# Kernel optimization log

Hardware: AMD Instinct MI355X
Metric: run time of the kernel (lower is better)

The kernel has to match this reference:

```python
import jax, jax.numpy as jnp
import numpy as np

NEG = -1000000000.0  # mask sentinel used by the torch module

def setup_inputs() -> dict:
    key = jax.random.key(0)
    k1, k2, k3, k4 = jax.random.split(key, 4)
    B, N, F_in, F_out = 8, 2048, 128, 64
    h = jax.random.normal(k1, (B, N, F_in), dtype=jnp.float32)
    adj_mask = jnp.where(jax.random.uniform(k2, (B, N, N)) < 0.7, 0.0, NEG).astype(jnp.float32)
    # xavier_uniform with gain=1.414
    g = 1.414
    limW = g * np.sqrt(6.0 / (F_in + F_out))
    W = jax.random.uniform(k3, (F_in, F_out), minval=-limW, maxval=limW, dtype=jnp.float32)
    lima = g * np.sqrt(6.0 / (2 * F_out + 1))
    a = jax.random.uniform(k4, (2 * F_out, 1), minval=-lima, maxval=lima, dtype=jnp.float32)
    return {"h": h, "adj_mask": adj_mask, "W": W, "a": a}

def reference(h, adj_mask, W, a):
    F_out = W.shape[1]
    wh = jnp.matmul(h, W)                       # [B, N, F_out]
    wh1 = jnp.matmul(wh, a[:F_out])             # [B, N, 1]
    wh2 = jnp.matmul(wh, a[F_out:])             # [B, N, 1]
    e = wh1 + jnp.swapaxes(wh2, 1, 2)           # [B, N, N] additive score
    e = jax.nn.leaky_relu(e, negative_slope=0.2)
    e = jnp.where(adj_mask == NEG, NEG, e)
    attention = jax.nn.softmax(e, axis=-1)      # dropout is identity in eval mode
    h_prime = jnp.matmul(attention, wh)         # [B, N, F_out]
    return jax.nn.elu(h_prime)
```

## Files before the change

### kernel.cpp

```cpp
#include <hip/hip_runtime.h>
#include <hip/hip_bf16.h>

#define BATCH 8
#define NN 2048
#define FIN 128
#define FOUT 64
#define ROWS_TOTAL (BATCH * NN)

typedef __attribute__((ext_vector_type(8))) short bf16x8;
typedef __attribute__((ext_vector_type(4))) float f32x4;
typedef __attribute__((ext_vector_type(8))) short short8;

__device__ inline short f2bf(float x) {
    __hip_bfloat16 b = __float2bfloat16(x);
    short s;
    __builtin_memcpy(&s, &b, 2);
    return s;
}

__device__ inline bf16x8 score8(float q, float4 w0, float4 w1, float4 a0, float4 a1) {
    float p[8];
    float e;
    e = q + w0.x; p[0] = __expf(fmaxf(e, 0.2f * e) + a0.x);
    e = q + w0.y; p[1] = __expf(fmaxf(e, 0.2f * e) + a0.y);
    e = q + w0.z; p[2] = __expf(fmaxf(e, 0.2f * e) + a0.z);
    e = q + w0.w; p[3] = __expf(fmaxf(e, 0.2f * e) + a0.w);
    e = q + w1.x; p[4] = __expf(fmaxf(e, 0.2f * e) + a1.x);
    e = q + w1.y; p[5] = __expf(fmaxf(e, 0.2f * e) + a1.y);
    e = q + w1.z; p[6] = __expf(fmaxf(e, 0.2f * e) + a1.z);
    e = q + w1.w; p[7] = __expf(fmaxf(e, 0.2f * e) + a1.w);
    bf16x8 r;
    #pragma unroll
    for (int i = 0; i < 8; ++i) r[i] = f2bf(p[i]);
    return r;
}

__global__ __launch_bounds__(256) void k1_proj(
        const float* __restrict__ h, const float* __restrict__ W,
        const float* __restrict__ a,
        short* __restrict__ whT, float* __restrict__ wh1, float* __restrict__ wh2) {
    const int tid  = threadIdx.x;
    const int lane = tid & 63;
    const int wid  = tid >> 6;
    const int gw   = blockIdx.x * 4 + wid;
    const int row0 = gw * 8;
    const int b    = row0 >> 11;
    const int rloc = row0 & (NN - 1);

    float acc[8] = {0.f,0.f,0.f,0.f,0.f,0.f,0.f,0.f};
    const float* hrow = h + (size_t)row0 * FIN;

    #pragma unroll 2
    for (int kc = 0; kc < FIN / 4; ++kc) {
        float wv0 = W[(4*kc + 0) * FOUT + lane];
        float wv1 = W[(4*kc + 1) * FOUT + lane];
        float wv2 = W[(4*kc + 2) * FOUT + lane];
        float wv3 = W[(4*kc + 3) * FOUT + lane];
        #pragma unroll
        for (int r = 0; r < 8; ++r) {
            float4 h4 = *(const float4*)(hrow + r * FIN + 4*kc);
            acc[r] = fmaf(h4.x, wv0, acc[r]);
            acc[r] = fmaf(h4.y, wv1, acc[r]);
            acc[r] = fmaf(h4.z, wv2, acc[r]);
            acc[r] = fmaf(h4.w, wv3, acc[r]);
        }
    }

    short8 st;
    #pragma unroll
    for (int r = 0; r < 8; ++r) st[r] = f2bf(acc[r]);
    *(short8*)(whT + ((size_t)b * FOUT + lane) * NN + rloc) = st;

    const float a1 = a[lane];
    const float a2 = a[FOUT + lane];
    #pragma unroll
    for (int r = 0; r < 8; ++r) {
        const int row = row0 + r;
        float v1 = acc[r] * a1;
        float v2 = acc[r] * a2;
        #pragma unroll
        for (int m = 32; m >= 1; m >>= 1) {
            v1 += __shfl_xor(v1, m, 64);
            v2 += __shfl_xor(v2, m, 64);
        }
        if (lane == 0) { wh1[row] = v1; wh2[row] = v2; }
    }
}

__global__ __launch_bounds__(256) void k2_attn(
        const float* __restrict__ adj, const short* __restrict__ whT,
        const float* __restrict__ wh1, const float* __restrict__ wh2,
        float* __restrict__ out) {
    __shared__ float lds_acc[4][16][FOUT];
    __shared__ float lds_l[4][16];

    const int tid  = threadIdx.x;
    const int lane = tid & 63;
    const int w    = tid >> 6;
    const int row0 = blockIdx.x * 16;
    const int b    = row0 >> 11;
    const int iloc = lane & 15;
    const int koff = (lane >> 4) * 8;

    const float* adjrow = adj + (size_t)(row0 + iloc) * NN;
    const float* wh2b   = wh2 + b * NN;
    const short* whTb   = whT + (size_t)b * FOUT * NN;
    const float  wh1v   = wh1[row0 + iloc];

    bf16x8 onesf, idxf;
    #pragma unroll
    for (int e = 0; e < 8; ++e) { onesf[e] = (short)0x3F80; idxf[e] = f2bf((float)iloc); }
    f32x4 rowM = {}, colM = {};
    rowM = __builtin_amdgcn_mfma_f32_16x16x32_bf16(idxf, onesf, rowM, 0, 0, 0);
    colM = __builtin_amdgcn_mfma_f32_16x16x32_bf16(onesf, idxf, colM, 0, 0, 0);
    int rmap[4], cmap[4];
    #pragma unroll
    for (int reg = 0; reg < 4; ++reg) {
        int r = (int)(rowM[reg] * 0.03125f + 0.5f);
        int c = (int)(colM[reg] * 0.03125f + 0.5f);
        rmap[reg] = min(max(r, 0), 15);
        cmap[reg] = min(max(c, 0), 15);
    }

    f32x4 acc[4] = {};
    f32x4 accl = {};

    const int base = w * 32 + koff;

    float4 aA0 = *(const float4*)(adjrow + base);
    float4 aA1 = *(const float4*)(adjrow + base + 4);
    float4 aB0 = *(const float4*)(adjrow + base + 128);
    float4 aB1 = *(const float4*)(adjrow + base + 132);
    float4 wA0 = *(const float4*)(wh2b + base);
    float4 wA1 = *(const float4*)(wh2b + base + 4);
    float4 wB0 = *(const float4*)(wh2b + base + 128);
    float4 wB1 = *(const float4*)(wh2b + base + 132);

    #pragma unroll
    for (int k = 0; k < 8; ++k) {
        const int jA = base + k * 256;
        const int jB = jA + 128;

        bf16x8 bfA[4], bfB[4];
        #pragma unroll
        for (int ft = 0; ft < 4; ++ft) {
            const short* rp = whTb + (size_t)(ft * 16 + iloc) * NN;
            bfA[ft] = *(const bf16x8*)(rp + jA);
            bfB[ft] = *(const bf16x8*)(rp + jB);
        }

        float4 naA0 = aA0, naA1 = aA1, naB0 = aB0, naB1 = aB1;
        float4 nwA0 = wA0, nwA1 = wA1, nwB0 = wB0, nwB1 = wB1;
        if (k < 7) {
            const float* qA = adjrow + jA + 256;
            const float* qW = wh2b + jA + 256;
            naA0 = *(const float4*)(qA);
            naA1 = *(const float4*)(qA + 4);
            naB0 = *(const float4*)(qA + 128);
            naB1 = *(const float4*)(qA + 132);
            nwA0 = *(const float4*)(qW);
            nwA1 = *(const float4*)(qW + 4);
            nwB0 = *(const float4*)(qW + 128);
            nwB1 = *(const float4*)(qW + 132);
        }

        bf16x8 afA = score8(wh1v, wA0, wA1, aA0, aA1);
        bf16x8 afB = score8(wh1v, wB0, wB1, aB0, aB1);

        accl = __builtin_amdgcn_mfma_f32_16x16x32_bf16(afA, onesf, accl, 0, 0, 0);
        #pragma unroll
        for (int ft = 0; ft < 4; ++ft)
            acc[ft] = __builtin_amdgcn_mfma_f32_16x16x32_bf16(afA, bfA[ft], acc[ft], 0, 0, 0);
        accl = __builtin_amdgcn_mfma_f32_16x16x32_bf16(afB, onesf, accl, 0, 0, 0);
        #pragma unroll
        for (int ft = 0; ft < 4; ++ft)
            acc[ft] = __builtin_amdgcn_mfma_f32_16x16x32_bf16(afB, bfB[ft], acc[ft], 0, 0, 0);

        aA0 = naA0; aA1 = naA1; aB0 = naB0; aB1 = naB1;
        wA0 = nwA0; wA1 = nwA1; wB0 = nwB0; wB1 = nwB1;
    }

    #pragma unroll
    for (int ft = 0; ft < 4; ++ft)
        #pragma unroll
        for (int reg = 0; reg < 4; ++reg)
            lds_acc[w][rmap[reg]][ft * 16 + cmap[reg]] = acc[ft][reg];
    #pragma unroll
    for (int reg = 0; reg < 4; ++reg)
        if (cmap[reg] == 0) lds_l[w][rmap[reg]] = accl[reg];
    __syncthreads();

    const int f  = tid & 63;
    const int r0 = tid >> 6;
    #pragma unroll
    for (int rr = 0; rr < 4; ++rr) {
        const int r = r0 * 4 + rr;
        float s = lds_acc[0][r][f] + lds_acc[1][r][f] + lds_acc[2][r][f] + lds_acc[3][r][f];
        float l = lds_l[0][r] + lds_l[1][r] + lds_l[2][r] + lds_l[3][r];
        float v = s / l;
        out[(size_t)(row0 + r) * FOUT + f] = (v > 0.f) ? v : (__expf(v) - 1.f);
    }
}

extern "C" void kernel_launch(void* const* d_in, const int* in_sizes, int n_in,
                              void* d_out, int out_size, void* d_ws, size_t ws_size,
                              hipStream_t stream) {
    const float* h   = (const float*)d_in[0];
    const float* adj = (const float*)d_in[1];
    const float* W   = (const float*)d_in[2];
    const float* a   = (const float*)d_in[3];
    float* out = (float*)d_out;

    short* whT = (short*)d_ws;
    float* wh1 = (float*)(whT + (size_t)BATCH * FOUT * NN);
    float* wh2 = wh1 + ROWS_TOTAL;

    k1_proj<<<ROWS_TOTAL / 32, 256, 0, stream>>>(h, W, a, whT, wh1, wh2);
    k2_attn<<<ROWS_TOTAL / 16, 256, 0, stream>>>(adj, whT, wh1, wh2, out);
}
```

Before: 73.85 us.

## Split attention K-loop across eight waves per block instead of four

```diff
diff --git a/kernel.cpp b/kernel.cpp
--- a/kernel.cpp
+++ b/kernel.cpp
@@ -87,12 +87,12 @@
     }
 }
 
-__global__ __launch_bounds__(256) void k2_attn(
+__global__ __launch_bounds__(512, 4) void k2_attn(
         const float* __restrict__ adj, const short* __restrict__ whT,
         const float* __restrict__ wh1, const float* __restrict__ wh2,
         float* __restrict__ out) {
-    __shared__ float lds_acc[4][16][FOUT];
-    __shared__ float lds_l[4][16];
+    __shared__ float lds_acc[8][16][FOUT];
+    __shared__ float lds_l[8][16];
 
     const int tid  = threadIdx.x;
     const int lane = tid & 63;
@@ -127,57 +127,36 @@
 
     const int base = w * 32 + koff;
 
-    float4 aA0 = *(const float4*)(adjrow + base);
-    float4 aA1 = *(const float4*)(adjrow + base + 4);
-    float4 aB0 = *(const float4*)(adjrow + base + 128);
-    float4 aB1 = *(const float4*)(adjrow + base + 132);
-    float4 wA0 = *(const float4*)(wh2b + base);
-    float4 wA1 = *(const float4*)(wh2b + base + 4);
-    float4 wB0 = *(const float4*)(wh2b + base + 128);
-    float4 wB1 = *(const float4*)(wh2b + base + 132);
+    float4 a0 = *(const float4*)(adjrow + base);
+    float4 a1 = *(const float4*)(adjrow + base + 4);
+    float4 w0 = *(const float4*)(wh2b + base);
+    float4 w1 = *(const float4*)(wh2b + base + 4);
 
     #pragma unroll
     for (int k = 0; k < 8; ++k) {
-        const int jA = base + k * 256;
-        const int jB = jA + 128;
-
-        bf16x8 bfA[4], bfB[4];
-        #pragma unroll
-        for (int ft = 0; ft < 4; ++ft) {
-            const short* rp = whTb + (size_t)(ft * 16 + iloc) * NN;
-            bfA[ft] = *(const bf16x8*)(rp + jA);
-            bfB[ft] = *(const bf16x8*)(rp + jB);
-        }
-
-        float4 naA0 = aA0, naA1 = aA1, naB0 = aB0, naB1 = aB1;
-        float4 nwA0 = wA0, nwA1 = wA1, nwB0 = wB0, nwB1 = wB1;
+        const int j0 = base + k * 256;
+
+        bf16x8 bf[4];
+        #pragma unroll
+        for (int ft = 0; ft < 4; ++ft)
+            bf[ft] = *(const bf16x8*)(whTb + (size_t)(ft * 16 + iloc) * NN + j0);
+
+        float4 na0 = a0, na1 = a1, nw0 = w0, nw1 = w1;
         if (k < 7) {
-            const float* qA = adjrow + jA + 256;
-            const float* qW = wh2b + jA + 256;
-            naA0 = *(const float4*)(qA);
-            naA1 = *(const float4*)(qA + 4);
-            naB0 = *(const float4*)(qA + 128);
-            naB1 = *(const float4*)(qA + 132);
-            nwA0 = *(const float4*)(qW);
-            nwA1 = *(const float4*)(qW + 4);
-            nwB0 = *(const float4*)(qW + 128);
-            nwB1 = *(const float4*)(qW + 132);
-        }
-
-        bf16x8 afA = score8(wh1v, wA0, wA1, aA0, aA1);
-        bf16x8 afB = score8(wh1v, wB0, wB1, aB0, aB1);
-
-        accl = __builtin_amdgcn_mfma_f32_16x16x32_bf16(afA, onesf, accl, 0, 0, 0);
+            na0 = *(const float4*)(adjrow + j0 + 256);
+            na1 = *(const float4*)(adjrow + j0 + 260);
+            nw0 = *(const float4*)(wh2b + j0 + 256);
+            nw1 = *(const float4*)(wh2b + j0 + 260);
+        }
+
+        bf16x8 af = score8(wh1v, w0, w1, a0, a1);
+
+        accl = __builtin_amdgcn_mfma_f32_16x16x32_bf16(af, onesf, accl, 0, 0, 0);
         #pragma unroll
         for (int ft = 0; ft < 4; ++ft)
-            acc[ft] = __builtin_amdgcn_mfma_f32_16x16x32_bf16(afA, bfA[ft], acc[ft], 0, 0, 0);
-        accl = __builtin_amdgcn_mfma_f32_16x16x32_bf16(afB, onesf, accl, 0, 0, 0);
-        #pragma unroll
-        for (int ft = 0; ft < 4; ++ft)
-            acc[ft] = __builtin_amdgcn_mfma_f32_16x16x32_bf16(afB, bfB[ft], acc[ft], 0, 0, 0);
-
-        aA0 = naA0; aA1 = naA1; aB0 = naB0; aB1 = naB1;
-        wA0 = nwA0; wA1 = nwA1; wB0 = nwB0; wB1 = nwB1;
+            acc[ft] = __builtin_amdgcn_mfma_f32_16x16x32_bf16(af, bf[ft], acc[ft], 0, 0, 0);
+
+        a0 = na0; a1 = na1; w0 = nw0; w1 = nw1;
     }
 
     #pragma unroll
@@ -191,12 +170,16 @@
     __syncthreads();
 
     const int f  = tid & 63;
-    const int r0 = tid >> 6;
-    #pragma unroll
-    for (int rr = 0; rr < 4; ++rr) {
-        const int r = r0 * 4 + rr;
-        float s = lds_acc[0][r][f] + lds_acc[1][r][f] + lds_acc[2][r][f] + lds_acc[3][r][f];
-        float l = lds_l[0][r] + lds_l[1][r] + lds_l[2][r] + lds_l[3][r];
+    const int rh = tid >> 6;
+    #pragma unroll
+    for (int rr = 0; rr < 2; ++rr) {
+        const int r = rh * 2 + rr;
+        float s = 0.f, l = 0.f;
+        #pragma unroll
+        for (int ww = 0; ww < 8; ++ww) {
+            s += lds_acc[ww][r][f];
+            l += lds_l[ww][r];
+        }
         float v = s / l;
         out[(size_t)(row0 + r) * FOUT + f] = (v > 0.f) ? v : (__expf(v) - 1.f);
     }
@@ -216,5 +199,5 @@
     float* wh2 = wh1 + ROWS_TOTAL;
 
     k1_proj<<<ROWS_TOTAL / 32, 256, 0, stream>>>(h, W, a, whT, wh1, wh2);
-    k2_attn<<<ROWS_TOTAL / 16, 256, 0, stream>>>(adj, whT, wh1, wh2, out);
-}
+    k2_attn<<<ROWS_TOTAL / 16, 512, 0, stream>>>(adj, whT, wh1, wh2, out);
+}
```

Result: no change. 75.02 us (+1.6%).
